# Kernel tuning notes

Hardware: AMD Instinct MI355X
Metric: run time of the kernel (lower is better)

## Reference

```python
import jax, jax.numpy as jnp
import numpy as np

DEPTH = 9
SIGMA = 0.1
IN_SIGMA = 1.0
TOTAL_VARS = 2 ** DEPTH - 2  # 510 = sum of 2^(depth-d-1) for d in [0, depth-2]


def setup_inputs() -> dict:
    key = jax.random.key(0)
    N = 262144
    eps = jax.random.normal(key, (N, TOTAL_VARS), dtype=jnp.float32)
    return {"eps": eps, "N": N}


def reference(eps, N):
    # Collider binary tree sampling, vectorized per level.
    # Level d has 2^(DEPTH-d-1) variables; each variable's mean is the
    # join (sum) of a consecutive pair of parents from the previous level.
    outs = []
    offset = 0
    prev = None
    for d in range(DEPTH - 1):
        width = 2 ** (DEPTH - d - 1)
        e = jax.lax.dynamic_slice_in_dim(eps, offset, width, axis=1)  # [N, width]
        offset += width
        if d == 0:
            # root-level leaves: zero mean, in_sigma scale
            x = IN_SIGMA * e
        else:
            # join_link(parent_2k, parent_2k+1) = sum of adjacent pair
            m = prev[:, 0::2] + prev[:, 1::2]  # [N, width]
            x = m + SIGMA * e
        outs.append(x)
        prev = x
    # Flat level-major layout, same ordering as torch samples_list concatenated.
    return jnp.concatenate(outs, axis=1)  # [N, TOTAL_VARS]
```

## Files before the change

### kernel.cpp

```cpp
#include <hip/hip_runtime.h>


#define TOTAL_VARS 510
#define SIGMA 0.1f

__global__ __launch_bounds__(256) void collider_kernel(
    const float* __restrict__ eps,
    float* __restrict__ out,
    int N)
{
    __shared__ __align__(16) float lds[4 * 1020];

    const int tid  = (int)threadIdx.x;
    const int wave = tid >> 6;
    const int lane = tid & 63;

    const size_t pair = (size_t)blockIdx.x * 4 + wave;
    const float* __restrict__ gin = eps + pair * 1020;
    float* __restrict__ gout      = out + pair * 1020;
    float* lw = lds + wave * 1020;

    const float4* __restrict__ g4 = reinterpret_cast<const float4*>(gin);
    float4* l4 = reinterpret_cast<float4*>(lw);
#pragma unroll
    for (int c = 0; c < 4; ++c) {
        const int idx = c * 64 + lane;
        if (idx < 255) l4[idx] = g4[idx];
    }

#pragma unroll
    for (int rr = 0; rr < 2; ++rr) {
        float* row = lw + rr * TOTAL_VARS;

        const float2 a01 = *reinterpret_cast<const float2*>(row + 4 * lane);
        const float2 a23 = *reinterpret_cast<const float2*>(row + 4 * lane + 2);

        const float2 e1 = *reinterpret_cast<const float2*>(row + 256 + 2 * lane);
        const float x1a = a01.x + a01.y + SIGMA * e1.x;
        const float x1b = a23.x + a23.y + SIGMA * e1.y;
        float2 o1; o1.x = x1a; o1.y = x1b;
        *reinterpret_cast<float2*>(row + 256 + 2 * lane) = o1;

        const float e2 = row[384 + lane];
        float prev = x1a + x1b + SIGMA * e2;
        row[384 + lane] = prev;

#pragma unroll
        for (int d = 3; d < 8; ++d) {
            const int w   = 256 >> d;
            const int off = 512 - (512 >> d);
            const float a = __shfl(prev, 2 * lane);
            const float b = __shfl(prev, 2 * lane + 1);
            float e = 0.0f;
            if (lane < w) e = row[off + lane];
            const float v = a + b + SIGMA * e;
            if (lane < w) row[off + lane] = v;
            prev = v;
        }
    }

#pragma unroll
    for (int c = 0; c < 4; ++c) {
        const int idx = c * 64 + lane;
        if (idx < 255) *reinterpret_cast<float4*>(gout + 4 * idx) = l4[idx];
    }
}

extern "C" void kernel_launch(void* const* d_in, const int* in_sizes, int n_in,
                              void* d_out, int out_size, void* d_ws, size_t ws_size,
                              hipStream_t stream) {
    const float* eps = (const float*)d_in[0];
    float* out = (float*)d_out;
    const int N = in_sizes[0] / TOTAL_VARS;

    const int pairs = N / 2;
    const int blocks = pairs / 4;
    collider_kernel<<<blocks, 256, 0, stream>>>(eps, out, N);
}
```

Before: 201.3 us.

## Use persistent grid-stride waves with register prefetch and nontemporal loads/stores

```diff
diff --git a/kernel.cpp b/kernel.cpp
--- a/kernel.cpp
+++ b/kernel.cpp
@@ -2,67 +2,93 @@
 
 
 #define TOTAL_VARS 510
+#define PAIR_FLOATS 1020
 #define SIGMA 0.1f
+#define MEMFENCE() asm volatile("" ::: "memory")
+
+typedef float f4 __attribute__((ext_vector_type(4)));
 
 __global__ __launch_bounds__(256) void collider_kernel(
     const float* __restrict__ eps,
     float* __restrict__ out,
-    int N)
+    int npairs)
 {
-    __shared__ __align__(16) float lds[4 * 1020];
+    __shared__ __align__(16) float lds[4 * PAIR_FLOATS];
 
     const int tid  = (int)threadIdx.x;
     const int wave = tid >> 6;
     const int lane = tid & 63;
+    float* lw = lds + wave * PAIR_FLOATS;
+    f4* l4 = reinterpret_cast<f4*>(lw);
 
-    const size_t pair = (size_t)blockIdx.x * 4 + wave;
-    const float* __restrict__ gin = eps + pair * 1020;
-    float* __restrict__ gout      = out + pair * 1020;
-    float* lw = lds + wave * 1020;
+    const int gwave  = (int)blockIdx.x * 4 + wave;
+    const int nwaves = (int)gridDim.x * 4;
 
-    const float4* __restrict__ g4 = reinterpret_cast<const float4*>(gin);
-    float4* l4 = reinterpret_cast<float4*>(lw);
-#pragma unroll
-    for (int c = 0; c < 4; ++c) {
-        const int idx = c * 64 + lane;
-        if (idx < 255) l4[idx] = g4[idx];
+    f4 r0 = (f4)0.f, r1 = (f4)0.f, r2 = (f4)0.f, r3 = (f4)0.f;
+    int pair = gwave;
+    if (pair < npairs) {
+        const f4* g4 = reinterpret_cast<const f4*>(eps + (size_t)pair * PAIR_FLOATS);
+        r0 = __builtin_nontemporal_load(&g4[lane]);
+        r1 = __builtin_nontemporal_load(&g4[64 + lane]);
+        r2 = __builtin_nontemporal_load(&g4[128 + lane]);
+        if (lane < 63) r3 = __builtin_nontemporal_load(&g4[192 + lane]);
     }
 
-#pragma unroll
-    for (int rr = 0; rr < 2; ++rr) {
-        float* row = lw + rr * TOTAL_VARS;
+    for (; pair < npairs; pair += nwaves) {
+        l4[lane]       = r0;
+        l4[64 + lane]  = r1;
+        l4[128 + lane] = r2;
+        if (lane < 63) l4[192 + lane] = r3;
 
-        const float2 a01 = *reinterpret_cast<const float2*>(row + 4 * lane);
-        const float2 a23 = *reinterpret_cast<const float2*>(row + 4 * lane + 2);
-
-        const float2 e1 = *reinterpret_cast<const float2*>(row + 256 + 2 * lane);
-        const float x1a = a01.x + a01.y + SIGMA * e1.x;
-        const float x1b = a23.x + a23.y + SIGMA * e1.y;
-        float2 o1; o1.x = x1a; o1.y = x1b;
-        *reinterpret_cast<float2*>(row + 256 + 2 * lane) = o1;
-
-        const float e2 = row[384 + lane];
-        float prev = x1a + x1b + SIGMA * e2;
-        row[384 + lane] = prev;
+        const int nx = pair + nwaves;
+        if (nx < npairs) {
+            const f4* g4 = reinterpret_cast<const f4*>(eps + (size_t)nx * PAIR_FLOATS);
+            r0 = __builtin_nontemporal_load(&g4[lane]);
+            r1 = __builtin_nontemporal_load(&g4[64 + lane]);
+            r2 = __builtin_nontemporal_load(&g4[128 + lane]);
+            if (lane < 63) r3 = __builtin_nontemporal_load(&g4[192 + lane]);
+        }
+        MEMFENCE();
 
 #pragma unroll
-        for (int d = 3; d < 8; ++d) {
-            const int w   = 256 >> d;
-            const int off = 512 - (512 >> d);
-            const float a = __shfl(prev, 2 * lane);
-            const float b = __shfl(prev, 2 * lane + 1);
-            float e = 0.0f;
-            if (lane < w) e = row[off + lane];
-            const float v = a + b + SIGMA * e;
-            if (lane < w) row[off + lane] = v;
-            prev = v;
-        }
-    }
+        for (int rr = 0; rr < 2; ++rr) {
+            float* row = lw + rr * TOTAL_VARS;
+
+            const float2 a01 = *reinterpret_cast<const float2*>(row + 4 * lane);
+            const float2 a23 = *reinterpret_cast<const float2*>(row + 4 * lane + 2);
+
+            const float2 e1 = *reinterpret_cast<const float2*>(row + 256 + 2 * lane);
+            const float x1a = a01.x + a01.y + SIGMA * e1.x;
+            const float x1b = a23.x + a23.y + SIGMA * e1.y;
+            float2 o1; o1.x = x1a; o1.y = x1b;
+            *reinterpret_cast<float2*>(row + 256 + 2 * lane) = o1;
+
+            const float e2 = row[384 + lane];
+            float prev = x1a + x1b + SIGMA * e2;
+            row[384 + lane] = prev;
 
 #pragma unroll
-    for (int c = 0; c < 4; ++c) {
-        const int idx = c * 64 + lane;
-        if (idx < 255) *reinterpret_cast<float4*>(gout + 4 * idx) = l4[idx];
+            for (int d = 3; d < 8; ++d) {
+                const int w   = 256 >> d;
+                const int off = 512 - (512 >> d);
+                const float a = __shfl(prev, 2 * lane);
+                const float b = __shfl(prev, 2 * lane + 1);
+                float e = 0.0f;
+                if (lane < w) e = row[off + lane];
+                const float v = a + b + SIGMA * e;
+                if (lane < w) row[off + lane] = v;
+                prev = v;
+            }
+        }
+        MEMFENCE();
+
+        f4* gout4 = reinterpret_cast<f4*>(out + (size_t)pair * PAIR_FLOATS);
+#pragma unroll
+        for (int c = 0; c < 4; ++c) {
+            const int idx = c * 64 + lane;
+            if (idx < 255) __builtin_nontemporal_store(l4[idx], &gout4[idx]);
+        }
+        MEMFENCE();
     }
 }
 
@@ -72,8 +98,8 @@
     const float* eps = (const float*)d_in[0];
     float* out = (float*)d_out;
     const int N = in_sizes[0] / TOTAL_VARS;
+    const int npairs = N / 2;
 
-    const int pairs = N / 2;
-    const int blocks = pairs / 4;
-    collider_kernel<<<blocks, 256, 0, stream>>>(eps, out, N);
+    const int blocks = 2048;
+    collider_kernel<<<blocks, 256, 0, stream>>>(eps, out, npairs);
 }
```

Measured after the change: 218.2 us. 1.08x slower.
